# Performance work log

Hardware: AMD Instinct MI355X
Metric: run time of the kernel (lower is better)

The kernel has to match this reference:

```python
import jax, jax.numpy as jnp
import numpy as np

B, S, D, H = 4, 2048, 1024, 16
DH = D // H  # per-head depth = 64


def setup_inputs() -> dict:
    key = jax.random.key(0)
    kq, kk, kv = jax.random.split(key, 3)
    q = jax.random.normal(kq, (B, S, D), dtype=jnp.float32)
    k = jax.random.normal(kk, (B, S, D), dtype=jnp.float32)
    v = jax.random.normal(kv, (B, S, D), dtype=jnp.float32)
    # Standard look-ahead mask: 1.0 where attention is disallowed (j > i).
    mask = (1.0 - jnp.tril(jnp.ones((S, S), dtype=jnp.float32)))[None, None, :, :]
    return {"q": q, "k": k, "v": v, "mask": mask, "training": 0}


def _split_heads(x):
    # [B, S, D] -> [B, H, S, DH]
    b, s, _ = x.shape
    return x.reshape(b, s, H, DH).transpose(0, 2, 1, 3)


def reference(q, k, v, mask, training):
    qh, kh, vh = _split_heads(q), _split_heads(k), _split_heads(v)
    scale = 1.0 / jnp.sqrt(jnp.float32(DH))
    logits = jnp.einsum("bhqd,bhkd->bhqk", qh, kh) * scale  # [B,H,S,S]
    logits = logits + mask * (-1e9)
    weights = jax.nn.softmax(logits, axis=-1)
    attn = jnp.einsum("bhqk,bhkd->bhqd", weights, vh)  # [B,H,S,DH]
    out = attn.transpose(0, 2, 1, 3).reshape(q.shape[0], 1, -1, H * DH)  # [B,1,S,D]
    return out
```

## Files before the change

### kernel.cpp

```cpp
#include <hip/hip_runtime.h>
#include <hip/hip_bf16.h>


constexpr int Ss = 2048, Dd = 1024, Hh = 16, DH = 64, Bb = 4;
constexpr float QSCALE = 0.125f * 1.44269504088896f;
constexpr float MFIX2 = 13.0f;
constexpr float MFIXF = 9.0f;

typedef _Float16 half2_t __attribute__((ext_vector_type(2)));
typedef _Float16 half4_t __attribute__((ext_vector_type(4)));
typedef _Float16 half8_t __attribute__((ext_vector_type(8)));
typedef __attribute__((ext_vector_type(4))) float floatx4;
typedef __attribute__((ext_vector_type(8))) short short8;

union H8 { half8_t v; half2_t h2[4]; };

__device__ __forceinline__ half2_t pk(float a, float b) {
  return __builtin_bit_cast(half2_t, __builtin_amdgcn_cvt_pkrtz(a, b));
}
__device__ __forceinline__ float fexp2(float x) {
#if __has_builtin(__builtin_amdgcn_exp2f)
  return __builtin_amdgcn_exp2f(x);
#else
  return __exp2f(x);
#endif
}
__device__ __forceinline__ unsigned short f2bf(float f) {
  union { float f; unsigned u; } x; x.f = f;
  unsigned r = x.u + 0x7FFFu + ((x.u >> 16) & 1u);
  return (unsigned short)(r >> 16);
}
__device__ __forceinline__ unsigned short f2bf_trunc(float f) {
  union { float f; unsigned u; } x; x.f = f;
  return (unsigned short)(x.u >> 16);
}
__device__ __forceinline__ void async_cp16(const unsigned short* g, unsigned short* l) {
  __builtin_amdgcn_global_load_lds(
      (const __attribute__((address_space(1))) unsigned int*)g,
      (__attribute__((address_space(3))) unsigned int*)l, 16, 0, 0);
}

__global__ __launch_bounds__(256)
void prep_kv(const float* __restrict__ Kg, const float* __restrict__ Vg,
             unsigned short* __restrict__ Kh, unsigned short* __restrict__ Vt) {
  __shared__ float tile[64][65];
  const int s0 = (int)blockIdx.x * 64;
  const int bh = (int)blockIdx.y;
  const int b = bh >> 4, h = bh & 15;
  const int t = threadIdx.x;
  const int sl = t >> 2, qtr = t & 3;

  const size_t inoff = ((size_t)(b * Ss + s0 + sl)) * Dd + h * DH + qtr * 16;
  const float* krow = Kg + inoff;
  const float* vrow = Vg + inoff;
  const int pout = (2 * (sl >> 5) + ((sl & 7) >> 2)) * 16 + ((sl >> 3) & 3) * 4 + (sl & 3);
  unsigned short* kout = Kh + ((size_t)bh * Ss + s0 + pout) * 64 + qtr * 16;

  #pragma unroll
  for (int i = 0; i < 2; ++i) {
    float4 k0 = ((const float4*)krow)[i * 2 + 0];
    float4 k1 = ((const float4*)krow)[i * 2 + 1];
    H8 o;
    o.h2[0] = pk(k0.x, k0.y); o.h2[1] = pk(k0.z, k0.w);
    o.h2[2] = pk(k1.x, k1.y); o.h2[3] = pk(k1.z, k1.w);
    *(half8_t*)(kout + i * 8) = o.v;
  }
  #pragma unroll
  for (int i = 0; i < 4; ++i) {
    float4 v = ((const float4*)vrow)[i];
    tile[sl][qtr * 16 + i * 4 + 0] = v.x;
    tile[sl][qtr * 16 + i * 4 + 1] = v.y;
    tile[sl][qtr * 16 + i * 4 + 2] = v.z;
    tile[sl][qtr * 16 + i * 4 + 3] = v.w;
  }
  __syncthreads();
  const int d = t >> 2, kc = t & 3;
  unsigned short* orow = Vt + ((size_t)bh * DH + d) * Ss + s0 + kc * 16;
  #pragma unroll
  for (int i = 0; i < 2; ++i) {
    H8 o;
    o.h2[0] = pk(tile[kc * 16 + i * 8 + 0][d], tile[kc * 16 + i * 8 + 1][d]);
    o.h2[1] = pk(tile[kc * 16 + i * 8 + 2][d], tile[kc * 16 + i * 8 + 3][d]);
    o.h2[2] = pk(tile[kc * 16 + i * 8 + 4][d], tile[kc * 16 + i * 8 + 5][d]);
    o.h2[3] = pk(tile[kc * 16 + i * 8 + 6][d], tile[kc * 16 + i * 8 + 7][d]);
    *(half8_t*)(orow + i * 8) = o.v;
  }
}

__global__ __launch_bounds__(256, 2)
void mha_fa7(const float* __restrict__ Qg, const unsigned short* __restrict__ Kh,
             const unsigned short* __restrict__ Vt, float* __restrict__ Og) {
  __shared__ __align__(16) unsigned short Kld[2][128 * 64];
  __shared__ __align__(16) unsigned short Vld[2][64 * 128];

  const int tid = threadIdx.x;
  const int wave = tid >> 6, lane = tid & 63;
  const int c = lane & 15, qd = lane >> 4;
  const int bh = (int)blockIdx.y;
  const int b = bh >> 4, h = bh & 15;

  const unsigned short* kbase = Kh + (size_t)bh * Ss * 64;
  const unsigned short* vbase = Vt + (size_t)bh * DH * Ss;
  float* obase = Og + (size_t)b * Ss * Dd + h * DH;

  auto stage = [&](int kt, int bufi) {
    const unsigned short* ktile = kbase + kt * 128 * 64;
    #pragma unroll
    for (int it = 0; it < 4; ++it) {
      int p = (it * 4 + wave) * 64 + lane;
      int r = p >> 3, pos = p & 7, j = pos ^ (r & 7);
      async_cp16(ktile + r * 64 + j * 8, &Kld[bufi][(it * 4 + wave) * 512]);
    }
    #pragma unroll
    for (int it = 0; it < 4; ++it) {
      int p = (it * 4 + wave) * 64 + lane;
      int d = p >> 4, c16 = p & 15;
      int j = (c16 & 8) | ((c16 ^ d) & 7);
      async_cp16(vbase + (size_t)d * Ss + kt * 128 + j * 8,
                 &Vld[bufi][(it * 4 + wave) * 512]);
    }
  };

  const half8_t ones8 = {(_Float16)1.f, (_Float16)1.f, (_Float16)1.f, (_Float16)1.f,
                         (_Float16)1.f, (_Float16)1.f, (_Float16)1.f, (_Float16)1.f};
  const int tiles[2] = {15 - (int)blockIdx.x, (int)blockIdx.x};

  for (int ti = 0; ti < 2; ++ti) {
    const int Q = tiles[ti];
    const int nkt = Q + 1;

    half8_t qf[2][2];
    #pragma unroll
    for (int mi = 0; mi < 2; ++mi) {
      const float* qr =
          Qg + ((size_t)b * Ss + Q * 128 + mi * 64 + wave * 16 + c) * Dd + h * DH;
      #pragma unroll
      for (int ks = 0; ks < 2; ++ks) {
        float4 a0 = ((const float4*)(qr + ks * 32 + qd * 8))[0];
        float4 a1 = ((const float4*)(qr + ks * 32 + qd * 8))[1];
        H8 f;
        f.h2[0] = pk(a0.x * QSCALE, a0.y * QSCALE);
        f.h2[1] = pk(a0.z * QSCALE, a0.w * QSCALE);
        f.h2[2] = pk(a1.x * QSCALE, a1.y * QSCALE);
        f.h2[3] = pk(a1.z * QSCALE, a1.w * QSCALE);
        qf[mi][ks] = f.v;
      }
    }

    floatx4 o_acc[2][4];
    floatx4 l_acc[2];
    #pragma unroll
    for (int mi = 0; mi < 2; ++mi) {
      #pragma unroll
      for (int f = 0; f < 4; ++f) o_acc[mi][f] = (floatx4){0.f, 0.f, 0.f, 0.f};
      l_acc[mi] = (floatx4){0.f, 0.f, 0.f, 0.f};
    }

    __syncthreads();
    stage(0, 0);

    for (int kt = 0; kt < nkt; ++kt) {
      __syncthreads();
      const int bufi = kt & 1;
      if (kt + 1 < nkt) stage(kt + 1, bufi ^ 1);

      const unsigned short* Kl = Kld[bufi];
      const unsigned short* Vl = Vld[bufi];

      #pragma unroll
      for (int kb = 0; kb < 2; ++kb) {
        const int kb0 = kt * 128 + kb * 64;
        if (kb0 > Q * 128 + 64 + wave * 16 + 15) continue;

        half8_t kf0[4], kf1[4];
        #pragma unroll
        for (int f = 0; f < 4; ++f) {
          int kk = kb * 64 + f * 16 + c;
          kf0[f] = *(const half8_t*)&Kl[kk * 64 + (qd ^ (c & 7)) * 8];
          kf1[f] = *(const half8_t*)&Kl[kk * 64 + ((4 + qd) ^ (c & 7)) * 8];
        }
        half8_t w8[4][2];
        #pragma unroll
        for (int f = 0; f < 4; ++f) {
          int rr = f * 16 + c;
          #pragma unroll
          for (int wnd = 0; wnd < 2; ++wnd) {
            int chi = kb * 8 + wnd * 4 + qd;
            int phys = (chi & 8) | ((chi ^ rr) & 7);
            w8[f][wnd] = *(const half8_t*)&Vl[rr * 128 + phys * 8];
          }
        }

        #pragma unroll
        for (int mi = 0; mi < 2; ++mi) {
          const int qlo = Q * 128 + mi * 64 + wave * 16;
          if (kb0 > qlo + 15) continue;

          floatx4 s[4];
          #pragma unroll
          for (int f = 0; f < 4; ++f) s[f] = (floatx4){0.f, 0.f, 0.f, 0.f};
          #pragma unroll
          for (int f = 0; f < 4; ++f) {
            s[f] = __builtin_amdgcn_mfma_f32_16x16x32_f16(kf0[f], qf[mi][0], s[f], 0, 0, 0);
            s[f] = __builtin_amdgcn_mfma_f32_16x16x32_f16(kf1[f], qf[mi][1], s[f], 0, 0, 0);
          }
          if (kb0 + 63 > qlo) {
            #pragma unroll
            for (int f = 0; f < 4; ++f) {
              int keyb = kb0 + ((f >> 1) << 5) + ((f & 1) << 2) + qd * 8;
              #pragma unroll
              for (int r = 0; r < 4; ++r)
                if (keyb + r > qlo + c) s[f][r] = -1e30f;
            }
          }
          half8_t p8[2];
          #pragma unroll
          for (int wnd = 0; wnd < 2; ++wnd) {
            H8 pp;
            pp.h2[0] = pk(fexp2(s[2 * wnd][0] - MFIX2), fexp2(s[2 * wnd][1] - MFIX2));
            pp.h2[1] = pk(fexp2(s[2 * wnd][2] - MFIX2), fexp2(s[2 * wnd][3] - MFIX2));
            pp.h2[2] = pk(fexp2(s[2 * wnd + 1][0] - MFIX2), fexp2(s[2 * wnd + 1][1] - MFIX2));
            pp.h2[3] = pk(fexp2(s[2 * wnd + 1][2] - MFIX2), fexp2(s[2 * wnd + 1][3] - MFIX2));
            p8[wnd] = pp.v;
          }
          #pragma unroll
          for (int fd = 0; fd < 4; ++fd) {
            #pragma unroll
            for (int wnd = 0; wnd < 2; ++wnd)
              o_acc[mi][fd] = __builtin_amdgcn_mfma_f32_16x16x32_f16(
                  p8[wnd], w8[fd][wnd], o_acc[mi][fd], 0, 0, 0);
          }
          #pragma unroll
          for (int wnd = 0; wnd < 2; ++wnd)
            l_acc[mi] = __builtin_amdgcn_mfma_f32_16x16x32_f16(p8[wnd], ones8, l_acc[mi], 0, 0, 0);
        }
      }
    }

    #pragma unroll
    for (int mi = 0; mi < 2; ++mi)
      #pragma unroll
      for (int r = 0; r < 4; ++r) {
        float inv = 1.f / l_acc[mi][r];
        size_t row = (size_t)(Q * 128 + mi * 64 + wave * 16 + qd * 4 + r);
        #pragma unroll
        for (int f = 0; f < 4; ++f)
          obase[row * Dd + f * 16 + c] = o_acc[mi][f][r] * inv;
      }
  }
}

__global__ __launch_bounds__(256, 4)
void mha_fwd(const float* __restrict__ Qg, const float* __restrict__ Kg,
             const float* __restrict__ Vg, float* __restrict__ Og) {
  __shared__ __align__(16) unsigned short Kldf[64 * 72];
  __shared__ __align__(16) unsigned short Vtldf[64 * 72];
  __shared__ __align__(16) unsigned short Pldf[4 * 16 * 72];
  const int tid = threadIdx.x, wave = tid >> 6, lane = tid & 63;
  const int c = lane & 15, qd = lane >> 4;
  const int qt = (Ss / 64 - 1) - (int)blockIdx.x;
  const int b = (int)blockIdx.y >> 4, h = (int)blockIdx.y & 15;
  const float* qbase = Qg + (size_t)b * Ss * Dd + h * DH;
  const float* kbase = Kg + (size_t)b * Ss * Dd + h * DH;
  const float* vbase = Vg + (size_t)b * Ss * Dd + h * DH;
  short8 qfrag[2];
  {
    const float* qr = qbase + (size_t)(qt * 64 + wave * 16 + c) * Dd + qd * 8;
    for (int ks = 0; ks < 2; ++ks) {
      float4 a0 = ((const float4*)(qr + ks * 32))[0];
      float4 a1 = ((const float4*)(qr + ks * 32))[1];
      short8 f;
      f[0] = (short)f2bf(a0.x * 0.125f); f[1] = (short)f2bf(a0.y * 0.125f);
      f[2] = (short)f2bf(a0.z * 0.125f); f[3] = (short)f2bf(a0.w * 0.125f);
      f[4] = (short)f2bf(a1.x * 0.125f); f[5] = (short)f2bf(a1.y * 0.125f);
      f[6] = (short)f2bf(a1.z * 0.125f); f[7] = (short)f2bf(a1.w * 0.125f);
      qfrag[ks] = f;
    }
  }
  floatx4 o_acc[4];
  for (int f = 0; f < 4; ++f) o_acc[f] = (floatx4){0.f, 0.f, 0.f, 0.f};
  float l_lane[4] = {0.f, 0.f, 0.f, 0.f};
  const int row_g = qt * 64 + wave * 16;
  const int pbase = wave * 16 * 72;
  for (int kt = 0; kt <= qt; ++kt) {
    __syncthreads();
    {
      const int r = tid >> 2, quarter = tid & 3;
      const float* krow = kbase + (size_t)(kt * 64 + r) * Dd + quarter * 16;
      const float* vrow = vbase + (size_t)(kt * 64 + r) * Dd + quarter * 16;
      for (int i = 0; i < 4; ++i) {
        float4 kv = ((const float4*)krow)[i];
        int col = quarter * 16 + i * 4;
        ushort4 kk;
        kk.x = f2bf(kv.x); kk.y = f2bf(kv.y); kk.z = f2bf(kv.z); kk.w = f2bf(kv.w);
        *(ushort4*)&Kldf[r * 72 + col] = kk;
        float4 vv = ((const float4*)vrow)[i];
        Vtldf[(col + 0) * 72 + r] = f2bf(vv.x);
        Vtldf[(col + 1) * 72 + r] = f2bf(vv.y);
        Vtldf[(col + 2) * 72 + r] = f2bf(vv.z);
        Vtldf[(col + 3) * 72 + r] = f2bf(vv.w);
      }
    }
    __syncthreads();
    floatx4 s_acc[4];
    for (int f = 0; f < 4; ++f) s_acc[f] = (floatx4){0.f, 0.f, 0.f, 0.f};
    for (int f = 0; f < 4; ++f)
      for (int ks = 0; ks < 2; ++ks) {
        short8 kf = *(const short8*)&Kldf[(f * 16 + c) * 72 + ks * 32 + qd * 8];
        s_acc[f] = __builtin_amdgcn_mfma_f32_16x16x32_bf16(qfrag[ks], kf, s_acc[f], 0, 0, 0);
      }
    if (kt == qt)
      for (int f = 0; f < 4; ++f) {
        int key = kt * 64 + f * 16 + c;
        for (int r = 0; r < 4; ++r)
          if (key > row_g + qd * 4 + r) s_acc[f][r] = -1e30f;
      }
    for (int f = 0; f < 4; ++f)
      for (int r = 0; r < 4; ++r) {
        float p = __expf(s_acc[f][r] - MFIXF);
        l_lane[r] += p;
        Pldf[pbase + (qd * 4 + r) * 72 + f * 16 + c] = f2bf_trunc(p);
      }
    short8 pfrag[2];
    pfrag[0] = *(const short8*)&Pldf[pbase + c * 72 + qd * 8];
    pfrag[1] = *(const short8*)&Pldf[pbase + c * 72 + 32 + qd * 8];
    for (int f = 0; f < 4; ++f)
      for (int ks = 0; ks < 2; ++ks) {
        short8 vf = *(const short8*)&Vtldf[(f * 16 + c) * 72 + ks * 32 + qd * 8];
        o_acc[f] = __builtin_amdgcn_mfma_f32_16x16x32_bf16(pfrag[ks], vf, o_acc[f], 0, 0, 0);
      }
  }
  float* obase = Og + (size_t)b * Ss * Dd + h * DH;
  for (int r = 0; r < 4; ++r) {
    float lv = l_lane[r];
    lv += __shfl_xor(lv, 1); lv += __shfl_xor(lv, 2);
    lv += __shfl_xor(lv, 4); lv += __shfl_xor(lv, 8);
    float inv_l = 1.f / lv;
    size_t rowoff = (size_t)(row_g + qd * 4 + r) * Dd;
    for (int f = 0; f < 4; ++f)
      obase[rowoff + f * 16 + c] = o_acc[f][r] * inv_l;
  }
}

extern "C" void kernel_launch(void* const* d_in, const int* in_sizes, int n_in,
                              void* d_out, int out_size, void* d_ws, size_t ws_size,
                              hipStream_t stream) {
  const float* q = (const float*)d_in[0];
  const float* k = (const float*)d_in[1];
  const float* v = (const float*)d_in[2];
  float* out = (float*)d_out;

  const size_t elems = (size_t)Bb * Hh * Ss * DH;
  if (ws_size >= 2 * elems * 2) {
    unsigned short* kh = (unsigned short*)d_ws;
    unsigned short* vt = kh + elems;
    prep_kv<<<dim3(Ss / 64, Bb * Hh), 256, 0, stream>>>(k, v, kh, vt);
    mha_fa7<<<dim3(8, Bb * Hh), 256, 0, stream>>>(q, kh, vt, out);
  } else {
    mha_fwd<<<dim3(Ss / 64, Bb * Hh), 256, 0, stream>>>(q, k, v, out);
  }
}
```

Baseline: 200.2 us.

## Pair adjacent query tiles per block to share K/V staging across both

Each block now handles two adjacent 128-row query tiles (2t and 2t+1) together. Every K/V tile is staged into LDS once and used by both query tiles, instead of two separate passes over K/V for a complementary pair of tiles. The grid is transposed so the head index is the fast dimension, and slots are mapped so heavy and light blocks interleave. In exchange, per-block work is unbalanced (pair work grows with t) and register pressure roughly doubles, since there are twice as many accumulators and Q fragments, which could cause spills at launch bounds (256,2).

```diff
diff --git a/kernel.cpp b/kernel.cpp
--- a/kernel.cpp
+++ b/kernel.cpp
@@ -88,7 +88,7 @@
 }
 
 __global__ __launch_bounds__(256, 2)
-void mha_fa7(const float* __restrict__ Qg, const unsigned short* __restrict__ Kh,
+void mha_fa8(const float* __restrict__ Qg, const unsigned short* __restrict__ Kh,
              const unsigned short* __restrict__ Vt, float* __restrict__ Og) {
   __shared__ __align__(16) unsigned short Kld[2][128 * 64];
   __shared__ __align__(16) unsigned short Vld[2][64 * 128];
@@ -96,8 +96,12 @@
   const int tid = threadIdx.x;
   const int wave = tid >> 6, lane = tid & 63;
   const int c = lane & 15, qd = lane >> 4;
-  const int bh = (int)blockIdx.y;
+  const int bh = (int)blockIdx.x;
   const int b = bh >> 4, h = bh & 15;
+  const int slot = (int)blockIdx.y;
+  const int t = (slot < 4) ? slot : 11 - slot;
+  const int Qt[2] = {2 * t + 1, 2 * t};
+  const int nkt = 2 * t + 2;
 
   const unsigned short* kbase = Kh + (size_t)bh * Ss * 64;
   const unsigned short* vbase = Vt + (size_t)bh * DH * Ss;
@@ -123,17 +127,14 @@
 
   const half8_t ones8 = {(_Float16)1.f, (_Float16)1.f, (_Float16)1.f, (_Float16)1.f,
                          (_Float16)1.f, (_Float16)1.f, (_Float16)1.f, (_Float16)1.f};
-  const int tiles[2] = {15 - (int)blockIdx.x, (int)blockIdx.x};
-
+
+  half8_t qf[2][2][2];
+  #pragma unroll
   for (int ti = 0; ti < 2; ++ti) {
-    const int Q = tiles[ti];
-    const int nkt = Q + 1;
-
-    half8_t qf[2][2];
     #pragma unroll
     for (int mi = 0; mi < 2; ++mi) {
       const float* qr =
-          Qg + ((size_t)b * Ss + Q * 128 + mi * 64 + wave * 16 + c) * Dd + h * DH;
+          Qg + ((size_t)b * Ss + Qt[ti] * 128 + mi * 64 + wave * 16 + c) * Dd + h * DH;
       #pragma unroll
       for (int ks = 0; ks < 2; ++ks) {
         float4 a0 = ((const float4*)(qr + ks * 32 + qd * 8))[0];
@@ -143,57 +144,60 @@
         f.h2[1] = pk(a0.z * QSCALE, a0.w * QSCALE);
         f.h2[2] = pk(a1.x * QSCALE, a1.y * QSCALE);
         f.h2[3] = pk(a1.z * QSCALE, a1.w * QSCALE);
-        qf[mi][ks] = f.v;
-      }
-    }
-
-    floatx4 o_acc[2][4];
-    floatx4 l_acc[2];
+        qf[ti][mi][ks] = f.v;
+      }
+    }
+  }
+
+  floatx4 o_acc[2][2][4];
+  floatx4 l_acc[2][2];
+  #pragma unroll
+  for (int ti = 0; ti < 2; ++ti)
     #pragma unroll
     for (int mi = 0; mi < 2; ++mi) {
       #pragma unroll
-      for (int f = 0; f < 4; ++f) o_acc[mi][f] = (floatx4){0.f, 0.f, 0.f, 0.f};
-      l_acc[mi] = (floatx4){0.f, 0.f, 0.f, 0.f};
-    }
-
+      for (int f = 0; f < 4; ++f) o_acc[ti][mi][f] = (floatx4){0.f, 0.f, 0.f, 0.f};
+      l_acc[ti][mi] = (floatx4){0.f, 0.f, 0.f, 0.f};
+    }
+
+  stage(0, 0);
+
+  for (int kt = 0; kt < nkt; ++kt) {
     __syncthreads();
-    stage(0, 0);
-
-    for (int kt = 0; kt < nkt; ++kt) {
-      __syncthreads();
-      const int bufi = kt & 1;
-      if (kt + 1 < nkt) stage(kt + 1, bufi ^ 1);
-
-      const unsigned short* Kl = Kld[bufi];
-      const unsigned short* Vl = Vld[bufi];
-
-      #pragma unroll
-      for (int kb = 0; kb < 2; ++kb) {
-        const int kb0 = kt * 128 + kb * 64;
-        if (kb0 > Q * 128 + 64 + wave * 16 + 15) continue;
-
-        half8_t kf0[4], kf1[4];
+    const int bufi = kt & 1;
+    if (kt + 1 < nkt) stage(kt + 1, bufi ^ 1);
+
+    const unsigned short* Kl = Kld[bufi];
+    const unsigned short* Vl = Vld[bufi];
+
+    #pragma unroll
+    for (int kb = 0; kb < 2; ++kb) {
+      const int kb0 = kt * 128 + kb * 64;
+
+      half8_t kf0[4], kf1[4];
+      #pragma unroll
+      for (int f = 0; f < 4; ++f) {
+        int kk = kb * 64 + f * 16 + c;
+        kf0[f] = *(const half8_t*)&Kl[kk * 64 + (qd ^ (c & 7)) * 8];
+        kf1[f] = *(const half8_t*)&Kl[kk * 64 + ((4 + qd) ^ (c & 7)) * 8];
+      }
+      half8_t w8[4][2];
+      #pragma unroll
+      for (int f = 0; f < 4; ++f) {
+        int rr = f * 16 + c;
         #pragma unroll
-        for (int f = 0; f < 4; ++f) {
-          int kk = kb * 64 + f * 16 + c;
-          kf0[f] = *(const half8_t*)&Kl[kk * 64 + (qd ^ (c & 7)) * 8];
-          kf1[f] = *(const half8_t*)&Kl[kk * 64 + ((4 + qd) ^ (c & 7)) * 8];
+        for (int wnd = 0; wnd < 2; ++wnd) {
+          int chi = kb * 8 + wnd * 4 + qd;
+          int phys = (chi & 8) | ((chi ^ rr) & 7);
+          w8[f][wnd] = *(const half8_t*)&Vl[rr * 128 + phys * 8];
         }
-        half8_t w8[4][2];
-        #pragma unroll
-        for (int f = 0; f < 4; ++f) {
-          int rr = f * 16 + c;
-          #pragma unroll
-          for (int wnd = 0; wnd < 2; ++wnd) {
-            int chi = kb * 8 + wnd * 4 + qd;
-            int phys = (chi & 8) | ((chi ^ rr) & 7);
-            w8[f][wnd] = *(const half8_t*)&Vl[rr * 128 + phys * 8];
-          }
-        }
-
+      }
+
+      #pragma unroll
+      for (int ti = 0; ti < 2; ++ti) {
         #pragma unroll
         for (int mi = 0; mi < 2; ++mi) {
-          const int qlo = Q * 128 + mi * 64 + wave * 16;
+          const int qlo = Qt[ti] * 128 + mi * 64 + wave * 16;
           if (kb0 > qlo + 15) continue;
 
           floatx4 s[4];
@@ -201,8 +205,8 @@
           for (int f = 0; f < 4; ++f) s[f] = (floatx4){0.f, 0.f, 0.f, 0.f};
           #pragma unroll
           for (int f = 0; f < 4; ++f) {
-            s[f] = __builtin_amdgcn_mfma_f32_16x16x32_f16(kf0[f], qf[mi][0], s[f], 0, 0, 0);
-            s[f] = __builtin_amdgcn_mfma_f32_16x16x32_f16(kf1[f], qf[mi][1], s[f], 0, 0, 0);
+            s[f] = __builtin_amdgcn_mfma_f32_16x16x32_f16(kf0[f], qf[ti][mi][0], s[f], 0, 0, 0);
+            s[f] = __builtin_amdgcn_mfma_f32_16x16x32_f16(kf1[f], qf[ti][mi][1], s[f], 0, 0, 0);
           }
           if (kb0 + 63 > qlo) {
             #pragma unroll
@@ -227,27 +231,30 @@
           for (int fd = 0; fd < 4; ++fd) {
             #pragma unroll
             for (int wnd = 0; wnd < 2; ++wnd)
-              o_acc[mi][fd] = __builtin_amdgcn_mfma_f32_16x16x32_f16(
-                  p8[wnd], w8[fd][wnd], o_acc[mi][fd], 0, 0, 0);
+              o_acc[ti][mi][fd] = __builtin_amdgcn_mfma_f32_16x16x32_f16(
+                  p8[wnd], w8[fd][wnd], o_acc[ti][mi][fd], 0, 0, 0);
           }
           #pragma unroll
           for (int wnd = 0; wnd < 2; ++wnd)
-            l_acc[mi] = __builtin_amdgcn_mfma_f32_16x16x32_f16(p8[wnd], ones8, l_acc[mi], 0, 0, 0);
+            l_acc[ti][mi] = __builtin_amdgcn_mfma_f32_16x16x32_f16(p8[wnd], ones8,
+                                                                   l_acc[ti][mi], 0, 0, 0);
         }
       }
     }
-
+  }
+
+  #pragma unroll
+  for (int ti = 0; ti < 2; ++ti)
     #pragma unroll
     for (int mi = 0; mi < 2; ++mi)
       #pragma unroll
       for (int r = 0; r < 4; ++r) {
-        float inv = 1.f / l_acc[mi][r];
-        size_t row = (size_t)(Q * 128 + mi * 64 + wave * 16 + qd * 4 + r);
+        float inv = 1.f / l_acc[ti][mi][r];
+        size_t row = (size_t)(Qt[ti] * 128 + mi * 64 + wave * 16 + qd * 4 + r);
         #pragma unroll
         for (int f = 0; f < 4; ++f)
-          obase[row * Dd + f * 16 + c] = o_acc[mi][f][r] * inv;
-      }
-  }
+          obase[row * Dd + f * 16 + c] = o_acc[ti][mi][f][r] * inv;
+      }
 }
 
 __global__ __launch_bounds__(256, 4)
@@ -355,7 +362,7 @@
     unsigned short* kh = (unsigned short*)d_ws;
     unsigned short* vt = kh + elems;
     prep_kv<<<dim3(Ss / 64, Bb * Hh), 256, 0, stream>>>(k, v, kh, vt);
-    mha_fa7<<<dim3(8, Bb * Hh), 256, 0, stream>>>(q, kh, vt, out);
+    mha_fa8<<<dim3(Bb * Hh, 8), 256, 0, stream>>>(q, kh, vt, out);
   } else {
     mha_fwd<<<dim3(Ss / 64, Bb * Hh), 256, 0, stream>>>(q, k, v, out);
   }
```

Measured after the change: 200.3 us. No clear change (+0.0%).
